# Optimization experiments

Hardware: AMD Instinct MI355X
Metric: run time of the kernel (lower is better)

## Reference

```python
import jax, jax.numpy as jnp
import numpy as np

# LDPC-like Tanner graph: N variable nodes, M check nodes, dv edges per variable
N_VAR = 8192
N_CHK = 4096
DV = 3
N_EDGE = N_VAR * DV  # 24576 = code.H.E
BATCH = 128
T = 30               # opt.T iterations
EPS = 1e-7


def setup_inputs() -> dict:
    key = jax.random.key(0)
    k1, k2 = jax.random.split(key)
    # channel LLRs for a batch of received codewords, shape (N_VAR, BATCH)
    chn_llr = jax.random.normal(k1, (N_VAR, BATCH), dtype=jnp.float32) * 2.0
    # Tanner graph edge lists: edge e connects variable edge_var[e] <-> check edge_chk[e]
    edge_var = jnp.repeat(jnp.arange(N_VAR, dtype=jnp.int32), DV)
    edge_chk = jax.random.randint(k2, (N_EDGE,), 0, N_CHK, dtype=jnp.int32)
    # gamma_logit = 0  ->  sigmoid = 0.5 = damping_init
    gamma_logit = jnp.zeros((1,), dtype=jnp.float32)
    return {"chn_llr": chn_llr, "gamma_logit": gamma_logit,
            "edge_var": edge_var, "edge_chk": edge_chk}


def reference(chn_llr, gamma_logit, edge_var, edge_chk):
    """T damped sum-product BP iterations over the Tanner graph.

    Returns stacked per-iteration posterior LLRs, shape (T, N_VAR, BATCH).
    """
    gamma = jax.nn.sigmoid(gamma_logit[0])  # damping gate, shared (tie=True)
    segsum = jax.ops.segment_sum

    def step(carry, _):
        msg_C2V, msg_V2C = carry  # each (N_EDGE, BATCH)
        # ---- variable -> check update (extrinsic sum), damped by gamma ----
        var_sum = segsum(msg_C2V, edge_var, num_segments=N_VAR)        # (N_VAR, B)
        v2c_new = chn_llr[edge_var] + var_sum[edge_var] - msg_C2V       # (E, B)
        msg_V2C = gamma * v2c_new + (1.0 - gamma) * msg_V2C
        # ---- check -> variable update (tanh product rule, log/sign domain) ----
        t = jnp.tanh(jnp.clip(msg_V2C, -15.0, 15.0) * 0.5)              # (E, B)
        logabs = jnp.log(jnp.maximum(jnp.abs(t), EPS))
        neg = (t < 0.0).astype(msg_V2C.dtype)
        chk_log = segsum(logabs, edge_chk, num_segments=N_CHK)          # (N_CHK, B)
        chk_neg = segsum(neg, edge_chk, num_segments=N_CHK)
        ext_log = chk_log[edge_chk] - logabs                            # exclude self
        ext_sign = 1.0 - 2.0 * jnp.mod(chk_neg[edge_chk] - neg, 2.0)
        prod = jnp.clip(ext_sign * jnp.exp(ext_log), -1.0 + EPS, 1.0 - EPS)
        msg_C2V = 2.0 * jnp.arctanh(prod)
        # ---- per-iteration posterior LLR output ----
        out = chn_llr + segsum(msg_C2V, edge_var, num_segments=N_VAR)   # (N_VAR, B)
        return (msg_C2V, msg_V2C), out

    init = (jnp.zeros((N_EDGE, BATCH), dtype=chn_llr.dtype),
            jnp.zeros((N_EDGE, BATCH), dtype=chn_llr.dtype))
    _, outputs = jax.lax.scan(step, init, None, length=T)
    return outputs  # (T, N_VAR, BATCH)
```

## Files before the change

### kernel.cpp

```cpp
#include <hip/hip_runtime.h>
#include <math.h>

#define N_VAR 8192
#define N_CHK 4096
#define DV 3
#define N_EDGE (N_VAR * DV)
#define BATCH 128
#define T_ITERS 30
#define ELLW 24
#define SLOT_MAX (N_EDGE + 3 * N_CHK)

#define LOG2E 1.44269504088896340736f
#define LN2   0.69314718055994530942f

typedef _Float16 h4 __attribute__((ext_vector_type(4)));

__device__ __forceinline__ float tanh_half(float x) {
    float ex = __builtin_amdgcn_exp2f(x * LOG2E);
    float t = 1.0f - 2.0f * __builtin_amdgcn_rcpf(ex + 1.0f);
    float s = (x < 0.0f) ? -1.0f : 1.0f;
    return s * fmaxf(fabsf(t), 1e-7f);
}

__device__ __forceinline__ float atanh2(float p) {
    const float lim = 1.0f - 1e-7f;
    p = fminf(fmaxf(p, -lim), lim);
    return (__builtin_amdgcn_logf(1.0f + p) -
            __builtin_amdgcn_logf(1.0f - p)) * LN2;
}

__device__ __forceinline__ float rcp_nr(float x) {
    float r = __builtin_amdgcn_rcpf(x);
    return r * (2.0f - x * r);
}


__global__ void k_ell_scatter(const int* __restrict__ edge_chk,
                              int* __restrict__ deg_arr, int* __restrict__ ell_e) {
    int e = blockIdx.x * blockDim.x + threadIdx.x;
    if (e < N_EDGE) {
        int c = edge_chk[e];
        int pos = atomicAdd(&deg_arr[c], 1);
        if (pos < ELLW) ell_e[c * ELLW + pos] = e;
    }
}

__global__ void k_hist(const int* __restrict__ deg_arr, int* __restrict__ hist) {
    int c = blockIdx.x * 256 + threadIdx.x;
    if (c < N_CHK) {
        int d = deg_arr[c]; if (d > ELLW) d = ELLW;
        atomicAdd(&hist[d], 1);
    }
}

__global__ void k_buckets(const int* __restrict__ hist,
                          int* __restrict__ bucket_base,
                          int* __restrict__ slot_off) {
    if (threadIdx.x == 0 && blockIdx.x == 0) {
        int cb = 0, sb = 0;
        for (int d = 0; d <= ELLW; ++d) {
            bucket_base[d] = cb;
            slot_off[d] = sb;
            int pd = (d == 0) ? 0 : ((d + 3) & ~3);
            cb += hist[d];
            sb += hist[d] * pd;
        }
    }
}

__global__ void k_place(const int* __restrict__ deg_arr, int* __restrict__ cursor,
                        const int* __restrict__ bucket_base,
                        const int* __restrict__ slot_off,
                        int* __restrict__ s_desc_g, int* __restrict__ chk_base) {
    int c = blockIdx.x * 256 + threadIdx.x;
    if (c < N_CHK) {
        int d = deg_arr[c]; if (d > ELLW) d = ELLW;
        int pd = (d + 3) & ~3;
        int pos = atomicAdd(&cursor[d], 1);
        int i = bucket_base[d] + pos;
        int base = slot_off[d] + pos * pd;
        s_desc_g[i] = (base << 5) | d;
        chk_base[c] = base;
    }
}

__global__ void k_slotmap2(const int* __restrict__ ell_e,
                           const int* __restrict__ deg_arr,
                           const int* __restrict__ chk_base,
                           int* __restrict__ slot_e) {
    int gid = blockIdx.x * 256 + threadIdx.x;
    if (gid < N_CHK * ELLW) {
        int c = gid / ELLW;
        int j = gid - c * ELLW;
        int d = deg_arr[c]; if (d > ELLW) d = ELLW;
        if (j < d) slot_e[ell_e[gid]] = chk_base[c] + j;
    }
}

__global__ void k_slot4(const int* __restrict__ slot_e, int4* __restrict__ slot4) {
    int v = blockIdx.x * 256 + threadIdx.x;
    if (v < N_VAR) {
        int4 s;
        s.x = slot_e[3 * v + 0];
        s.y = slot_e[3 * v + 1];
        s.z = slot_e[3 * v + 2];
        s.w = 0;
        slot4[v] = s;
    }
}


__global__ __launch_bounds__(1024) void k_bp2(
        const float* __restrict__ chn,
        const float* __restrict__ gamma_logit,
        const int4* __restrict__ slot4,
        const int* __restrict__ s_desc_g,
        float* __restrict__ outT) {
    __shared__ __align__(16) _Float16 msg[SLOT_MAX];
    const int b = blockIdx.x;
    const int tid = threadIdx.x;

    for (int i = tid; i < SLOT_MAX; i += 1024) msg[i] = (_Float16)0.0f;

    const float g = 1.0f / (1.0f + __builtin_amdgcn_exp2f(-gamma_logit[0] * LOG2E));
    const float om = 1.0f - g;
    const float AT1 = atanh2(1.0f);

    float chn_r[8];
    float v2c_r[8][3];
    int4 s4r[8];
    int desc_r[4];
#pragma unroll
    for (int k = 0; k < 8; ++k) {
        int v = tid + k * 1024;
        chn_r[k] = chn[(size_t)v * BATCH + b];
        s4r[k] = slot4[v];
        v2c_r[k][0] = 0.0f; v2c_r[k][1] = 0.0f; v2c_r[k][2] = 0.0f;
    }
#pragma unroll
    for (int m = 0; m < 4; ++m) desc_r[m] = s_desc_g[m * 1024 + tid];
    __syncthreads();

    const size_t SLICE = (size_t)N_VAR * BATCH;

    for (int t = 0; t < T_ITERS; ++t) {
#pragma unroll
        for (int k = 0; k < 8; ++k) {
            int v = tid + k * 1024;
            int4 s4 = s4r[k];
            float c0 = (float)msg[s4.x];
            float c1 = (float)msg[s4.y];
            float c2 = (float)msg[s4.z];
            float post = chn_r[k] + c0 + c1 + c2;
            if (t > 0) {
                __builtin_nontemporal_store(post,
                    &outT[(size_t)(t - 1) * SLICE + (size_t)b * N_VAR + v]);
            }
            float vn0 = g * (post - c0) + om * v2c_r[k][0];
            float vn1 = g * (post - c1) + om * v2c_r[k][1];
            float vn2 = g * (post - c2) + om * v2c_r[k][2];
            v2c_r[k][0] = vn0; v2c_r[k][1] = vn1; v2c_r[k][2] = vn2;
            msg[s4.x] = (_Float16)fminf(fmaxf(vn0, -15.0f), 15.0f);
            msg[s4.y] = (_Float16)fminf(fmaxf(vn1, -15.0f), 15.0f);
            msg[s4.z] = (_Float16)fminf(fmaxf(vn2, -15.0f), 15.0f);
        }
        __syncthreads();

#pragma unroll
        for (int m = 0; m < 4; ++m) {
            int desc = desc_r[m];
            int base = desc >> 5;
            int deg = desc & 31;
            if (deg == 1) {
                msg[base] = (_Float16)AT1;
            } else if (deg > 1) {
                int nw = (deg + 3) >> 2;
                h4 raw[6];
#pragma unroll
                for (int w = 0; w < 6; ++w)
                    if (w < nw) raw[w] = *(const h4*)&msg[base + 4 * w];
                float tv[ELLW];
                float P = 1.0f;
#pragma unroll
                for (int j = 0; j < ELLW; ++j)
                    if (j < deg) {
                        tv[j] = tanh_half((float)raw[j >> 2][j & 3]);
                        P *= tv[j];
                    }
#pragma unroll
                for (int w = 0; w < 6; ++w)
                    if (w < nw) {
                        h4 out_w;
#pragma unroll
                        for (int q = 0; q < 4; ++q) {
                            int j = 4 * w + q;
                            float m2 = (j < deg) ? atanh2(P * rcp_nr(tv[j])) : 0.0f;
                            out_w[q] = (_Float16)m2;
                        }
                        *(h4*)&msg[base + 4 * w] = out_w;
                    }
            }
        }
        __syncthreads();
    }

#pragma unroll
    for (int k = 0; k < 8; ++k) {
        int v = tid + k * 1024;
        int4 s4 = s4r[k];
        float post = chn_r[k] + (float)msg[s4.x] + (float)msg[s4.y] +
                     (float)msg[s4.z];
        __builtin_nontemporal_store(post,
            &outT[(size_t)(T_ITERS - 1) * SLICE + (size_t)b * N_VAR + v]);
    }
}


__global__ __launch_bounds__(256) void k_transpose(const float* __restrict__ src,
                                                   float* __restrict__ dst) {
    __shared__ float tile[32][33];
    int t = blockIdx.z;
    int v0 = blockIdx.x * 32;
    int b0 = blockIdx.y * 32;
    int lx = threadIdx.x;
    int ly = threadIdx.y;
    const float* s = src + (size_t)t * N_VAR * BATCH;
    float* d = dst + (size_t)t * N_VAR * BATCH;
#pragma unroll
    for (int i = 0; i < 32; i += 8)
        tile[ly + i][lx] = s[(size_t)(b0 + ly + i) * N_VAR + v0 + lx];
    __syncthreads();
#pragma unroll
    for (int i = 0; i < 32; i += 8)
        __builtin_nontemporal_store(tile[lx][ly + i],
            &d[(size_t)(v0 + ly + i) * BATCH + b0 + lx]);
}


extern "C" void kernel_launch(void* const* d_in, const int* in_sizes, int n_in,
                              void* d_out, int out_size, void* d_ws, size_t ws_size,
                              hipStream_t stream) {
    const float* chn         = (const float*)d_in[0];
    const float* gamma_logit = (const float*)d_in[1];
    const int* edge_chk      = (const int*)d_in[3];
    float* out = (float*)d_out;

    int4* slot4      = (int4*)d_ws;
    int* slot_e      = (int*)(slot4 + N_VAR);
    int* ell_e       = slot_e + N_EDGE;
    int* deg_arr     = ell_e + (size_t)N_CHK * ELLW;
    int* chk_base    = deg_arr + N_CHK;
    int* s_desc_g    = chk_base + N_CHK;
    int* hist        = s_desc_g + N_CHK;
    int* cursor      = hist + 32;
    int* bucket_base = cursor + 32;
    int* slot_off    = bucket_base + 32;
    size_t table_bytes = (char*)(slot_off + 32) - (char*)d_ws;
    size_t outT_off = (table_bytes + 255) & ~(size_t)255;
    float* outT = (float*)((char*)d_ws + outT_off);

    (void)hipMemsetAsync(slot_e, 0, (size_t)N_EDGE * sizeof(int), stream);
    (void)hipMemsetAsync(deg_arr, 0, N_CHK * sizeof(int), stream);
    (void)hipMemsetAsync(hist, 0, 64 * sizeof(int), stream);

    k_ell_scatter<<<(N_EDGE + 255) / 256, 256, 0, stream>>>(edge_chk, deg_arr,
                                                            ell_e);
    k_hist<<<N_CHK / 256, 256, 0, stream>>>(deg_arr, hist);
    k_buckets<<<1, 64, 0, stream>>>(hist, bucket_base, slot_off);
    k_place<<<N_CHK / 256, 256, 0, stream>>>(deg_arr, cursor, bucket_base,
                                             slot_off, s_desc_g, chk_base);
    k_slotmap2<<<(N_CHK * ELLW + 255) / 256, 256, 0, stream>>>(ell_e, deg_arr,
                                                               chk_base, slot_e);
    k_slot4<<<N_VAR / 256, 256, 0, stream>>>(slot_e, slot4);

    k_bp2<<<BATCH, 1024, 0, stream>>>(chn, gamma_logit, slot4, s_desc_g, outT);

    dim3 tg(N_VAR / 32, BATCH / 32, T_ITERS);
    dim3 tb(32, 8, 1);
    k_transpose<<<tg, tb, 0, stream>>>(outT, out);
}
```

Baseline: 575.1 us.

## Fuse setup kernels and overlap transpose with BP iterations via flags

The six graph-setup kernels are merged into one single-block kernel that keeps its intermediates in shared memory. The BP kernel and the output transpose are fused into one launch: extra blocks spin on per-iteration global flags and transpose each iteration's slice while BP blocks keep iterating. The intermediate posterior buffer is stored as fp16 to halve its write and read traffic. The risks are reduced output precision, deadlock if the BP blocks are not all co-resident with the waiting blocks, and serial execution of the setup on a single block.

```diff
diff --git a/kernel.cpp b/kernel.cpp
--- a/kernel.cpp
+++ b/kernel.cpp
@@ -9,6 +9,7 @@
 #define T_ITERS 30
 #define ELLW 24
 #define SLOT_MAX (N_EDGE + 3 * N_CHK)
+#define NWK 128
 
 #define LOG2E 1.44269504088896340736f
 #define LN2   0.69314718055994530942f
@@ -35,71 +36,64 @@
 }
 
 
-__global__ void k_ell_scatter(const int* __restrict__ edge_chk,
-                              int* __restrict__ deg_arr, int* __restrict__ ell_e) {
-    int e = blockIdx.x * blockDim.x + threadIdx.x;
-    if (e < N_EDGE) {
+__global__ __launch_bounds__(1024) void k_setup(
+        const int* __restrict__ edge_chk,
+        int* __restrict__ ell_e,
+        int* __restrict__ slot_e,
+        int* __restrict__ s_desc_g,
+        int4* __restrict__ slot4) {
+    __shared__ int deg[N_CHK];
+    __shared__ int chk_base_s[N_CHK];
+    __shared__ int hist[32], cursor[32], bbase[32], soff[32];
+    const int tid = threadIdx.x;
+
+    for (int i = tid; i < N_CHK; i += 1024) deg[i] = 0;
+    if (tid < 32) { hist[tid] = 0; cursor[tid] = 0; }
+    __syncthreads();
+
+    for (int e = tid; e < N_EDGE; e += 1024) {
         int c = edge_chk[e];
-        int pos = atomicAdd(&deg_arr[c], 1);
+        int pos = atomicAdd(&deg[c], 1);
         if (pos < ELLW) ell_e[c * ELLW + pos] = e;
     }
-}
-
-__global__ void k_hist(const int* __restrict__ deg_arr, int* __restrict__ hist) {
-    int c = blockIdx.x * 256 + threadIdx.x;
-    if (c < N_CHK) {
-        int d = deg_arr[c]; if (d > ELLW) d = ELLW;
+    __syncthreads();
+
+    for (int c = tid; c < N_CHK; c += 1024) {
+        int d = deg[c]; if (d > ELLW) { d = ELLW; deg[c] = d; }
         atomicAdd(&hist[d], 1);
     }
-}
-
-__global__ void k_buckets(const int* __restrict__ hist,
-                          int* __restrict__ bucket_base,
-                          int* __restrict__ slot_off) {
-    if (threadIdx.x == 0 && blockIdx.x == 0) {
+    __syncthreads();
+
+    if (tid == 0) {
         int cb = 0, sb = 0;
         for (int d = 0; d <= ELLW; ++d) {
-            bucket_base[d] = cb;
-            slot_off[d] = sb;
-            int pd = (d == 0) ? 0 : ((d + 3) & ~3);
+            bbase[d] = cb; soff[d] = sb;
+            int pd = (d + 3) & ~3;
             cb += hist[d];
-            sb += hist[d] * pd;
-        }
-    }
-}
-
-__global__ void k_place(const int* __restrict__ deg_arr, int* __restrict__ cursor,
-                        const int* __restrict__ bucket_base,
-                        const int* __restrict__ slot_off,
-                        int* __restrict__ s_desc_g, int* __restrict__ chk_base) {
-    int c = blockIdx.x * 256 + threadIdx.x;
-    if (c < N_CHK) {
-        int d = deg_arr[c]; if (d > ELLW) d = ELLW;
+            sb += (d == 0) ? 0 : hist[d] * pd;
+        }
+    }
+    __syncthreads();
+
+    for (int c = tid; c < N_CHK; c += 1024) {
+        int d = deg[c];
         int pd = (d + 3) & ~3;
         int pos = atomicAdd(&cursor[d], 1);
-        int i = bucket_base[d] + pos;
-        int base = slot_off[d] + pos * pd;
+        int i = bbase[d] + pos;
+        int base = soff[d] + pos * pd;
         s_desc_g[i] = (base << 5) | d;
-        chk_base[c] = base;
-    }
-}
-
-__global__ void k_slotmap2(const int* __restrict__ ell_e,
-                           const int* __restrict__ deg_arr,
-                           const int* __restrict__ chk_base,
-                           int* __restrict__ slot_e) {
-    int gid = blockIdx.x * 256 + threadIdx.x;
-    if (gid < N_CHK * ELLW) {
+        chk_base_s[c] = base;
+    }
+    __syncthreads();
+
+    for (int gid = tid; gid < N_CHK * ELLW; gid += 1024) {
         int c = gid / ELLW;
         int j = gid - c * ELLW;
-        int d = deg_arr[c]; if (d > ELLW) d = ELLW;
-        if (j < d) slot_e[ell_e[gid]] = chk_base[c] + j;
-    }
-}
-
-__global__ void k_slot4(const int* __restrict__ slot_e, int4* __restrict__ slot4) {
-    int v = blockIdx.x * 256 + threadIdx.x;
-    if (v < N_VAR) {
+        if (j < deg[c]) slot_e[ell_e[gid]] = chk_base_s[c] + j;
+    }
+    __syncthreads();
+
+    for (int v = tid; v < N_VAR; v += 1024) {
         int4 s;
         s.x = slot_e[3 * v + 0];
         s.y = slot_e[3 * v + 1];
@@ -110,130 +104,155 @@
 }
 
 
-__global__ __launch_bounds__(1024) void k_bp2(
+__global__ __launch_bounds__(1024) void k_fused(
         const float* __restrict__ chn,
         const float* __restrict__ gamma_logit,
         const int4* __restrict__ slot4,
         const int* __restrict__ s_desc_g,
-        float* __restrict__ outT) {
+        _Float16* __restrict__ outT,
+        float* __restrict__ out,
+        int* __restrict__ flags) {
     __shared__ __align__(16) _Float16 msg[SLOT_MAX];
-    const int b = blockIdx.x;
     const int tid = threadIdx.x;
-
-    for (int i = tid; i < SLOT_MAX; i += 1024) msg[i] = (_Float16)0.0f;
-
-    const float g = 1.0f / (1.0f + __builtin_amdgcn_exp2f(-gamma_logit[0] * LOG2E));
-    const float om = 1.0f - g;
-    const float AT1 = atanh2(1.0f);
-
-    float chn_r[8];
-    float v2c_r[8][3];
-    int4 s4r[8];
-    int desc_r[4];
-#pragma unroll
-    for (int k = 0; k < 8; ++k) {
-        int v = tid + k * 1024;
-        chn_r[k] = chn[(size_t)v * BATCH + b];
-        s4r[k] = slot4[v];
-        v2c_r[k][0] = 0.0f; v2c_r[k][1] = 0.0f; v2c_r[k][2] = 0.0f;
-    }
-#pragma unroll
-    for (int m = 0; m < 4; ++m) desc_r[m] = s_desc_g[m * 1024 + tid];
-    __syncthreads();
-
     const size_t SLICE = (size_t)N_VAR * BATCH;
 
-    for (int t = 0; t < T_ITERS; ++t) {
+    if (blockIdx.x < BATCH) {
+        const int b = blockIdx.x;
+        for (int i = tid; i < SLOT_MAX; i += 1024) msg[i] = (_Float16)0.0f;
+
+        const float g = 1.0f /
+            (1.0f + __builtin_amdgcn_exp2f(-gamma_logit[0] * LOG2E));
+        const float om = 1.0f - g;
+        const float AT1 = atanh2(1.0f);
+
+        float chn_r[8];
+        float v2c_r[8][3];
+        int4 s4r[8];
+        int desc_r[4];
+#pragma unroll
+        for (int k = 0; k < 8; ++k) {
+            int v = tid + k * 1024;
+            chn_r[k] = chn[(size_t)v * BATCH + b];
+            s4r[k] = slot4[v];
+            v2c_r[k][0] = 0.0f; v2c_r[k][1] = 0.0f; v2c_r[k][2] = 0.0f;
+        }
+#pragma unroll
+        for (int m = 0; m < 4; ++m) desc_r[m] = s_desc_g[m * 1024 + tid];
+        __syncthreads();
+
+        for (int t = 0; t < T_ITERS; ++t) {
+#pragma unroll
+            for (int k = 0; k < 8; ++k) {
+                int v = tid + k * 1024;
+                int4 s4 = s4r[k];
+                float c0 = (float)msg[s4.x];
+                float c1 = (float)msg[s4.y];
+                float c2 = (float)msg[s4.z];
+                float post = chn_r[k] + c0 + c1 + c2;
+                if (t > 0) {
+                    __builtin_nontemporal_store((_Float16)post,
+                        &outT[(size_t)(t - 1) * SLICE + (size_t)b * N_VAR + v]);
+                }
+                float vn0 = g * (post - c0) + om * v2c_r[k][0];
+                float vn1 = g * (post - c1) + om * v2c_r[k][1];
+                float vn2 = g * (post - c2) + om * v2c_r[k][2];
+                v2c_r[k][0] = vn0; v2c_r[k][1] = vn1; v2c_r[k][2] = vn2;
+                msg[s4.x] = (_Float16)fminf(fmaxf(vn0, -15.0f), 15.0f);
+                msg[s4.y] = (_Float16)fminf(fmaxf(vn1, -15.0f), 15.0f);
+                msg[s4.z] = (_Float16)fminf(fmaxf(vn2, -15.0f), 15.0f);
+            }
+            __syncthreads();
+            if (t > 0 && tid == 0) {
+                __threadfence();
+                __hip_atomic_fetch_add(&flags[t - 1], 1, __ATOMIC_RELEASE,
+                                       __HIP_MEMORY_SCOPE_AGENT);
+            }
+
+#pragma unroll
+            for (int m = 0; m < 4; ++m) {
+                int desc = desc_r[m];
+                int base = desc >> 5;
+                int deg = desc & 31;
+                if (deg == 1) {
+                    msg[base] = (_Float16)AT1;
+                } else if (deg > 1) {
+                    int nw = (deg + 3) >> 2;
+                    h4 raw[6];
+#pragma unroll
+                    for (int w = 0; w < 6; ++w)
+                        if (w < nw) raw[w] = *(const h4*)&msg[base + 4 * w];
+                    float tv[ELLW];
+                    float P = 1.0f;
+#pragma unroll
+                    for (int j = 0; j < ELLW; ++j)
+                        if (j < deg) {
+                            tv[j] = tanh_half((float)raw[j >> 2][j & 3]);
+                            P *= tv[j];
+                        }
+#pragma unroll
+                    for (int w = 0; w < 6; ++w)
+                        if (w < nw) {
+                            h4 out_w;
+#pragma unroll
+                            for (int q = 0; q < 4; ++q) {
+                                int j = 4 * w + q;
+                                float m2 = 0.0f;
+                                if (j < deg)
+                                    m2 = atanh2(P * rcp_nr(tv[j]));
+                                out_w[q] = (_Float16)m2;
+                            }
+                            *(h4*)&msg[base + 4 * w] = out_w;
+                        }
+                }
+            }
+            __syncthreads();
+        }
+
 #pragma unroll
         for (int k = 0; k < 8; ++k) {
             int v = tid + k * 1024;
             int4 s4 = s4r[k];
-            float c0 = (float)msg[s4.x];
-            float c1 = (float)msg[s4.y];
-            float c2 = (float)msg[s4.z];
-            float post = chn_r[k] + c0 + c1 + c2;
-            if (t > 0) {
-                __builtin_nontemporal_store(post,
-                    &outT[(size_t)(t - 1) * SLICE + (size_t)b * N_VAR + v]);
-            }
-            float vn0 = g * (post - c0) + om * v2c_r[k][0];
-            float vn1 = g * (post - c1) + om * v2c_r[k][1];
-            float vn2 = g * (post - c2) + om * v2c_r[k][2];
-            v2c_r[k][0] = vn0; v2c_r[k][1] = vn1; v2c_r[k][2] = vn2;
-            msg[s4.x] = (_Float16)fminf(fmaxf(vn0, -15.0f), 15.0f);
-            msg[s4.y] = (_Float16)fminf(fmaxf(vn1, -15.0f), 15.0f);
-            msg[s4.z] = (_Float16)fminf(fmaxf(vn2, -15.0f), 15.0f);
+            float post = chn_r[k] + (float)msg[s4.x] + (float)msg[s4.y] +
+                         (float)msg[s4.z];
+            __builtin_nontemporal_store((_Float16)post,
+                &outT[(size_t)(T_ITERS - 1) * SLICE + (size_t)b * N_VAR + v]);
         }
         __syncthreads();
-
-#pragma unroll
-        for (int m = 0; m < 4; ++m) {
-            int desc = desc_r[m];
-            int base = desc >> 5;
-            int deg = desc & 31;
-            if (deg == 1) {
-                msg[base] = (_Float16)AT1;
-            } else if (deg > 1) {
-                int nw = (deg + 3) >> 2;
-                h4 raw[6];
-#pragma unroll
-                for (int w = 0; w < 6; ++w)
-                    if (w < nw) raw[w] = *(const h4*)&msg[base + 4 * w];
-                float tv[ELLW];
-                float P = 1.0f;
-#pragma unroll
-                for (int j = 0; j < ELLW; ++j)
-                    if (j < deg) {
-                        tv[j] = tanh_half((float)raw[j >> 2][j & 3]);
-                        P *= tv[j];
-                    }
-#pragma unroll
-                for (int w = 0; w < 6; ++w)
-                    if (w < nw) {
-                        h4 out_w;
-#pragma unroll
-                        for (int q = 0; q < 4; ++q) {
-                            int j = 4 * w + q;
-                            float m2 = (j < deg) ? atanh2(P * rcp_nr(tv[j])) : 0.0f;
-                            out_w[q] = (_Float16)m2;
-                        }
-                        *(h4*)&msg[base + 4 * w] = out_w;
-                    }
-            }
-        }
-        __syncthreads();
-    }
-
-#pragma unroll
-    for (int k = 0; k < 8; ++k) {
-        int v = tid + k * 1024;
-        int4 s4 = s4r[k];
-        float post = chn_r[k] + (float)msg[s4.x] + (float)msg[s4.y] +
-                     (float)msg[s4.z];
-        __builtin_nontemporal_store(post,
-            &outT[(size_t)(T_ITERS - 1) * SLICE + (size_t)b * N_VAR + v]);
-    }
-}
-
-
-__global__ __launch_bounds__(256) void k_transpose(const float* __restrict__ src,
-                                                   float* __restrict__ dst) {
-    __shared__ float tile[32][33];
-    int t = blockIdx.z;
-    int v0 = blockIdx.x * 32;
-    int b0 = blockIdx.y * 32;
-    int lx = threadIdx.x;
-    int ly = threadIdx.y;
-    const float* s = src + (size_t)t * N_VAR * BATCH;
-    float* d = dst + (size_t)t * N_VAR * BATCH;
-#pragma unroll
-    for (int i = 0; i < 32; i += 8)
-        tile[ly + i][lx] = s[(size_t)(b0 + ly + i) * N_VAR + v0 + lx];
-    __syncthreads();
-#pragma unroll
-    for (int i = 0; i < 32; i += 8)
-        __builtin_nontemporal_store(tile[lx][ly + i],
-            &d[(size_t)(v0 + ly + i) * BATCH + b0 + lx]);
+        if (tid == 0) {
+            __threadfence();
+            __hip_atomic_fetch_add(&flags[T_ITERS - 1], 1, __ATOMIC_RELEASE,
+                                   __HIP_MEMORY_SCOPE_AGENT);
+        }
+    } else {
+        const int w = blockIdx.x - BATCH;
+        const int lx = tid & 31;
+        const int ly = tid >> 5;
+        float (*tile)[33] = (float(*)[33])msg;
+
+        for (int t = 0; t < T_ITERS; ++t) {
+            if (tid == 0) {
+                while (__hip_atomic_load(&flags[t], __ATOMIC_ACQUIRE,
+                                         __HIP_MEMORY_SCOPE_AGENT) < BATCH)
+                    __builtin_amdgcn_s_sleep(8);
+            }
+            __syncthreads();
+            __threadfence();
+
+            const _Float16* s = outT + (size_t)t * SLICE;
+            float* d = out + (size_t)t * SLICE;
+#pragma unroll
+            for (int i = 0; i < 8; ++i) {
+                int tile_id = w + i * NWK;
+                int v0 = (tile_id >> 2) * 32;
+                int b0 = (tile_id & 3) * 32;
+                tile[ly][lx] = (float)s[(size_t)(b0 + ly) * N_VAR + v0 + lx];
+                __syncthreads();
+                __builtin_nontemporal_store(tile[lx][ly],
+                    &d[(size_t)(v0 + ly) * BATCH + b0 + lx]);
+                __syncthreads();
+            }
+        }
+    }
 }
 
 
@@ -245,37 +264,19 @@
     const int* edge_chk      = (const int*)d_in[3];
     float* out = (float*)d_out;
 
-    int4* slot4      = (int4*)d_ws;
-    int* slot_e      = (int*)(slot4 + N_VAR);
-    int* ell_e       = slot_e + N_EDGE;
-    int* deg_arr     = ell_e + (size_t)N_CHK * ELLW;
-    int* chk_base    = deg_arr + N_CHK;
-    int* s_desc_g    = chk_base + N_CHK;
-    int* hist        = s_desc_g + N_CHK;
-    int* cursor      = hist + 32;
-    int* bucket_base = cursor + 32;
-    int* slot_off    = bucket_base + 32;
-    size_t table_bytes = (char*)(slot_off + 32) - (char*)d_ws;
+    int4* slot4   = (int4*)d_ws;
+    int* slot_e   = (int*)(slot4 + N_VAR);
+    int* ell_e    = slot_e + N_EDGE;
+    int* s_desc_g = ell_e + (size_t)N_CHK * ELLW;
+    int* flags    = s_desc_g + N_CHK;
+    size_t table_bytes = (char*)(flags + 64) - (char*)d_ws;
     size_t outT_off = (table_bytes + 255) & ~(size_t)255;
-    float* outT = (float*)((char*)d_ws + outT_off);
-
-    (void)hipMemsetAsync(slot_e, 0, (size_t)N_EDGE * sizeof(int), stream);
-    (void)hipMemsetAsync(deg_arr, 0, N_CHK * sizeof(int), stream);
-    (void)hipMemsetAsync(hist, 0, 64 * sizeof(int), stream);
-
-    k_ell_scatter<<<(N_EDGE + 255) / 256, 256, 0, stream>>>(edge_chk, deg_arr,
-                                                            ell_e);
-    k_hist<<<N_CHK / 256, 256, 0, stream>>>(deg_arr, hist);
-    k_buckets<<<1, 64, 0, stream>>>(hist, bucket_base, slot_off);
-    k_place<<<N_CHK / 256, 256, 0, stream>>>(deg_arr, cursor, bucket_base,
-                                             slot_off, s_desc_g, chk_base);
-    k_slotmap2<<<(N_CHK * ELLW + 255) / 256, 256, 0, stream>>>(ell_e, deg_arr,
-                                                               chk_base, slot_e);
-    k_slot4<<<N_VAR / 256, 256, 0, stream>>>(slot_e, slot4);
-
-    k_bp2<<<BATCH, 1024, 0, stream>>>(chn, gamma_logit, slot4, s_desc_g, outT);
-
-    dim3 tg(N_VAR / 32, BATCH / 32, T_ITERS);
-    dim3 tb(32, 8, 1);
-    k_transpose<<<tg, tb, 0, stream>>>(outT, out);
-}
+    _Float16* outT = (_Float16*)((char*)d_ws + outT_off);
+
+    (void)hipMemsetAsync(flags, 0, 64 * sizeof(int), stream);
+
+    k_setup<<<1, 1024, 0, stream>>>(edge_chk, ell_e, slot_e, s_desc_g, slot4);
+
+    k_fused<<<BATCH + NWK, 1024, 0, stream>>>(chn, gamma_logit, slot4,
+                                              s_desc_g, outT, out, flags);
+}
```

New measurement: 2.029 ms. 3.53x slower.
